# Kernel optimization log

Hardware: AMD Instinct MI355X
Metric: run time of the kernel (lower is better)

The kernel has to match this reference:

```python
import jax, jax.numpy as jnp
import numpy as np

H = 1024          # hidden_size
NH = 16           # num_attention_heads
HD = H // NH      # attention_head_size = 64
B, S = 8, 1024
LN_EPS = 1e-12


def setup_inputs() -> dict:
    key = jax.random.key(0)
    ks = jax.random.split(key, 12)
    sc = 0.02
    return {
        "input_tensor": jax.random.normal(ks[0], (B, S, H), dtype=jnp.float32),
        "attention_mask": jnp.zeros((B, S), dtype=jnp.float32),
        # LinearMem params (quantization disabled -> plain Linear, torch layout [out,in])
        "Wq": jax.random.normal(ks[1], (H, H), dtype=jnp.float32) * sc,
        "bq": jnp.zeros((H,), dtype=jnp.float32),
        "Wk": jax.random.normal(ks[2], (H, H), dtype=jnp.float32) * sc,
        "bk": jnp.zeros((H,), dtype=jnp.float32),
        "Wv": jax.random.normal(ks[3], (H, H), dtype=jnp.float32) * sc,
        "bv": jnp.zeros((H,), dtype=jnp.float32),
        "Wo": jax.random.normal(ks[4], (H, H), dtype=jnp.float32) * sc,
        "bo": jnp.zeros((H,), dtype=jnp.float32),
        "ln_gamma": jnp.ones((H,), dtype=jnp.float32),
        "ln_beta": jnp.zeros((H,), dtype=jnp.float32),
    }


def _heads(x):  # [B,S,H] -> [B,NH,S,HD]
    return x.reshape(B, S, NH, HD).transpose(0, 2, 1, 3)


def reference(input_tensor, attention_mask, Wq, bq, Wk, bk, Wv, bv, Wo, bo, ln_gamma, ln_beta):
    # Q/K/V projections (LinearMem with quantization disabled == Linear)
    q = _heads(jnp.einsum('bsh,oh->bso', input_tensor, Wq) + bq)
    k = _heads(jnp.einsum('bsh,oh->bso', input_tensor, Wk) + bk)
    v = _heads(jnp.einsum('bsh,oh->bso', input_tensor, Wv) + bv)
    scores = jnp.einsum('bnqd,bnkd->bnqk', q, k) / np.float32(np.sqrt(HD))
    scores = scores + attention_mask[:, None, None, :]  # additive mask [B,1,1,S]
    probs = jax.nn.softmax(scores, axis=-1)  # dropout = identity in eval
    ctx = jnp.einsum('bnqk,bnkd->bnqd', probs, v)
    ctx = ctx.transpose(0, 2, 1, 3).reshape(B, S, H)
    # output projection + residual LayerNorm (eps=1e-12)
    out = jnp.einsum('bsh,oh->bso', ctx, Wo) + bo
    resid = out + input_tensor
    mu = jnp.mean(resid, axis=-1, keepdims=True)
    var = jnp.mean(jnp.square(resid - mu), axis=-1, keepdims=True)
    return (resid - mu) * jax.lax.rsqrt(var + LN_EPS) * ln_gamma + ln_beta
```

## Files before the change

### kernel.cpp

```cpp
#include <hip/hip_runtime.h>

#define NHh 16

typedef unsigned short ushortT;
typedef __attribute__((ext_vector_type(8))) short short8;
typedef __attribute__((ext_vector_type(4))) float floatx4;

__device__ __forceinline__ ushortT f2bf(float x) {
    union { float f; unsigned int u; } cv; cv.f = x;
    unsigned int u = cv.u;
    unsigned int r = u + 0x7fffu + ((u >> 16) & 1u);
    return (ushortT)(r >> 16);
}

__device__ __forceinline__ unsigned pack2_trunc(float a, float b) {
    union { float f; unsigned u; } ua, ub;
    ua.f = a; ub.f = b;
    return (ub.u & 0xffff0000u) | (ua.u >> 16);
}

__device__ __forceinline__ void gload_lds16(const ushortT* g, ushortT* l) {
    __builtin_amdgcn_global_load_lds(
        (const __attribute__((address_space(1))) void*)g,
        (__attribute__((address_space(3))) void*)l, 16, 0, 0);
}

__global__ __launch_bounds__(256) void cvt_x(const float* __restrict__ in,
                                             ushortT* __restrict__ out, int n4) {
    int i = blockIdx.x * 256 + threadIdx.x;
    if (i >= n4) return;
    float4 f = ((const float4*)in)[i];
    uint2 o;
    o.x = (unsigned)f2bf(f.x) | ((unsigned)f2bf(f.y) << 16);
    o.y = (unsigned)f2bf(f.z) | ((unsigned)f2bf(f.w) << 16);
    ((uint2*)out)[i] = o;
}

__global__ __launch_bounds__(256) void cvt_w(const float* __restrict__ W0, const float* __restrict__ W1,
                                             const float* __restrict__ W2, const float* __restrict__ W3,
                                             ushortT* __restrict__ o0, ushortT* __restrict__ o1,
                                             ushortT* __restrict__ o2, ushortT* __restrict__ o3, int n4) {
    int z = blockIdx.y;
    const float* in = (z == 0) ? W0 : (z == 1) ? W1 : (z == 2) ? W2 : W3;
    ushortT* out = (z == 0) ? o0 : (z == 1) ? o1 : (z == 2) ? o2 : o3;
    int i = blockIdx.x * 256 + threadIdx.x;
    if (i >= n4) return;
    float4 f = ((const float4*)in)[i];
    uint2 o;
    o.x = (unsigned)f2bf(f.x) | ((unsigned)f2bf(f.y) << 16);
    o.y = (unsigned)f2bf(f.z) | ((unsigned)f2bf(f.w) << 16);
    ((uint2*)out)[i] = o;
}

__device__ __forceinline__ short8 lds_frag(const ushortT* tb, int row, int ks, int qd) {
    int rowblk = row >> 4;
    int r = row & 15;
    int c2 = qd ^ ((r >> 3) << 1);
    return *(const short8*)((const char*)tb + rowblk * 2048 + ks * 1024 + r * 64 + c2 * 16);
}

__global__ __launch_bounds__(512, 2) void qkv256(
        const ushortT* __restrict__ X,
        const ushortT* __restrict__ W0, const ushortT* __restrict__ W1, const ushortT* __restrict__ W2,
        const float* __restrict__ b0, const float* __restrict__ b1, const float* __restrict__ b2,
        ushortT* __restrict__ Qo, ushortT* __restrict__ Ko, ushortT* __restrict__ Vo) {
    __shared__ __align__(16) ushortT As[2 * 16384];
    __shared__ __align__(16) ushortT Bs[2 * 16384];

    const int l = blockIdx.x;
    const int z = l >> 7;
    const int idx = l & 127;
    const int tid = threadIdx.x;
    const int lane = tid & 63;
    const int w = tid >> 6;
    const int wr = w >> 2;
    const int wc = w & 3;
    const int qd = lane >> 4;
    const int ln = lane & 15;

    const ushortT* Ap; const ushortT* Bp;
    int arow0, brow0;
    if (z == 2) { Ap = W2; arow0 = (idx & 3) * 256; Bp = X; brow0 = (idx >> 2) * 256; }
    else { Ap = X; arow0 = (idx >> 2) * 256; Bp = (z == 0) ? W0 : W1; brow0 = (idx & 3) * 256; }

    floatx4 acc[8][4];
#pragma unroll
    for (int i = 0; i < 8; i++)
#pragma unroll
        for (int j = 0; j < 4; j++) acc[i][j] = (floatx4){0.f, 0.f, 0.f, 0.f};

    auto STAGE = [&](int cursor) {
        int kt = cursor >> 2;
        if (kt >= 16) return;
        int h = cursor & 3;
        int buf = kt & 1;
        int k0 = kt << 6;
        const ushortT* G = (h < 2) ? Ap : Bp;
        int row0 = (h < 2) ? arow0 : brow0;
        ushortT* L = (h < 2) ? (As + buf * 16384) : (Bs + buf * 16384);
        int half = h & 1;
#pragma unroll
        for (int j = 0; j < 2; j++) {
            int o = half * 16384 + j * 8192 + tid * 16;
            int rowblk = o >> 11;
            int colblk = (o >> 10) & 1;
            int r = (o >> 6) & 15;
            int c2 = ((o >> 4) & 3) ^ ((r >> 3) << 1);
            gload_lds16(G + (size_t)(row0 + rowblk * 16 + r) * 1024 + k0 + colblk * 32 + c2 * 8,
                        (ushortT*)((char*)L + o));
        }
    };

    for (int c = 0; c < 7; c++) STAGE(c);
    asm volatile("s_waitcnt vmcnt(6)" ::: "memory");
    __builtin_amdgcn_s_barrier();

    short8 afr[4][2], bfr[2][2];
    int cursor = 7;
    for (int T = 0; T < 16; T++) {
        const ushortT* Ab = As + (T & 1) * 16384;
        const ushortT* Bb = Bs + (T & 1) * 16384;
#pragma unroll
        for (int ph = 0; ph < 4; ph++) {
            const int mq = ph >> 1, nq = ph & 1;
#pragma unroll
            for (int ni = 0; ni < 2; ni++)
#pragma unroll
                for (int ks = 0; ks < 2; ks++)
                    bfr[ni][ks] = lds_frag(Bb, nq * 128 + ni * 64 + wc * 16 + ln, ks, qd);
            if (nq == 0) {
#pragma unroll
                for (int mi = 0; mi < 4; mi++)
#pragma unroll
                    for (int ks = 0; ks < 2; ks++)
                        afr[mi][ks] = lds_frag(Ab, (mq * 4 + mi) * 32 + wr * 16 + ln, ks, qd);
            }
            STAGE(cursor); ++cursor;
            __builtin_amdgcn_s_barrier();
            asm volatile("s_waitcnt lgkmcnt(0)" ::: "memory");
            __builtin_amdgcn_s_setprio(1);
#pragma unroll
            for (int mi = 0; mi < 4; mi++)
#pragma unroll
                for (int ni = 0; ni < 2; ni++)
#pragma unroll
                    for (int ks = 0; ks < 2; ks++)
                        acc[mq * 4 + mi][nq * 2 + ni] =
                            __builtin_amdgcn_mfma_f32_16x16x32_bf16(afr[mi][ks], bfr[ni][ks],
                                                                    acc[mq * 4 + mi][nq * 2 + ni], 0, 0, 0);
            __builtin_amdgcn_s_setprio(0);
            if (ph == 3) {
                if (T < 14) { asm volatile("s_waitcnt vmcnt(6)" ::: "memory"); }
                else        { asm volatile("s_waitcnt vmcnt(0)" ::: "memory"); }
            }
            __builtin_amdgcn_s_barrier();
        }
    }

    if (z == 2) {
        floatx4 bv4[8];
#pragma unroll
        for (int mi = 0; mi < 8; mi++)
            bv4[mi] = *(const floatx4*)(b2 + arow0 + mi * 32 + wr * 16 + qd * 4);
#pragma unroll
        for (int ni = 0; ni < 4; ni++) {
            int n = brow0 + ni * 64 + wc * 16 + ln;
            int bb = n >> 10, s = n & 1023;
#pragma unroll
            for (int mi = 0; mi < 8; mi++) {
#pragma unroll
                for (int r2 = 0; r2 < 4; r2++) {
                    int dim = arow0 + mi * 32 + wr * 16 + qd * 4 + r2;
                    int hh = dim >> 6, dd = dim & 63;
                    Vo[((size_t)(bb * NHh + hh) * 64 + dd) * 1024 + s] =
                        f2bf(acc[mi][ni][r2] + bv4[mi][r2]);
                }
            }
        }
    } else {
        ushortT* Out = z ? Ko : Qo;
        const float* bias = z ? b1 : b0;
#pragma unroll
        for (int ni = 0; ni < 4; ni++) {
            int n = brow0 + ni * 64 + wc * 16 + ln;
            float bb = bias[n];
            int h = n >> 6, d = n & 63;
#pragma unroll
            for (int mi = 0; mi < 8; mi++) {
#pragma unroll
                for (int r2 = 0; r2 < 4; r2++) {
                    int m = arow0 + mi * 32 + wr * 16 + qd * 4 + r2;
                    int b = m >> 10, s = m & 1023;
                    Out[(size_t)((b * NHh + h) * 1024 + s) * 64 + d] =
                        f2bf(acc[mi][ni][r2] + bb);
                }
            }
        }
    }
}

__global__ __launch_bounds__(256) void oproj_gemm(const ushortT* __restrict__ A,
        const ushortT* __restrict__ Wt, const float* __restrict__ bias, float* __restrict__ Pj) {
    __shared__ ushortT As[128 * 32];
    __shared__ ushortT Bs[128 * 32];
    const int l = blockIdx.x;
    const int m0 = (l & 63) * 128;
    const int n0 = (l >> 6) * 128;
    const int tid = threadIdx.x;
    const int lane = tid & 63;
    const int w = tid >> 6;
    const int qd = lane >> 4;
    const int ln = lane & 15;
    const int RM = (w >> 1) * 64;
    const int RN = (w & 1) * 64;

    floatx4 acc[4][4];
#pragma unroll
    for (int i = 0; i < 4; i++)
#pragma unroll
        for (int j = 0; j < 4; j++) acc[i][j] = (floatx4){0.f, 0.f, 0.f, 0.f};

    const int c0 = tid, c1 = tid + 256;
    for (int k0 = 0; k0 < 1024; k0 += 32) {
        gload_lds16(A + (size_t)(m0 + (c0 >> 2)) * 1024 + k0 + (c0 & 3) * 8, As + c0 * 8);
        gload_lds16(A + (size_t)(m0 + (c1 >> 2)) * 1024 + k0 + (c1 & 3) * 8, As + c1 * 8);
        gload_lds16(Wt + (size_t)(n0 + (c0 >> 2)) * 1024 + k0 + (c0 & 3) * 8, Bs + c0 * 8);
        gload_lds16(Wt + (size_t)(n0 + (c1 >> 2)) * 1024 + k0 + (c1 & 3) * 8, Bs + c1 * 8);
        __syncthreads();
        short8 af[4], bf8[4];
#pragma unroll
        for (int i = 0; i < 4; i++) af[i] = *(const short8*)&As[(RM + i * 16 + ln) * 32 + qd * 8];
#pragma unroll
        for (int j = 0; j < 4; j++) bf8[j] = *(const short8*)&Bs[(RN + j * 16 + ln) * 32 + qd * 8];
#pragma unroll
        for (int i = 0; i < 4; i++)
#pragma unroll
            for (int j = 0; j < 4; j++)
                acc[i][j] = __builtin_amdgcn_mfma_f32_16x16x32_bf16(af[i], bf8[j], acc[i][j], 0, 0, 0);
        __syncthreads();
    }

#pragma unroll
    for (int j = 0; j < 4; j++) {
        int n = n0 + RN + j * 16 + ln;
        float bb = bias[n];
#pragma unroll
        for (int i = 0; i < 4; i++) {
#pragma unroll
            for (int r2 = 0; r2 < 4; r2++) {
                int m = m0 + RM + i * 16 + qd * 4 + r2;
                Pj[(size_t)m * 1024 + n] = acc[i][j][r2] + bb;
            }
        }
    }
}

__global__ __launch_bounds__(256, 2) void attn_kernel(const ushortT* __restrict__ Q,
        const ushortT* __restrict__ K, const ushortT* __restrict__ Vg_t,
        const float* __restrict__ mask, ushortT* __restrict__ ctx) {
    __shared__ __align__(16) ushortT Ks[128 * 64];
    __shared__ __align__(16) ushortT Vt[64 * 128];
    __shared__ __align__(16) ushortT Ps[4][64 * 72];

    const int tid = threadIdx.x;
    const int lane = tid & 63;
    const int w = tid >> 6;
    const int qd = lane >> 4;
    const int ln = lane & 15;
    const int l = blockIdx.x;
    const int bh = l & 127;
    const int b = bh >> 4;
    const int h = bh & 15;
    const int qb = l >> 7;

    const ushortT* Qg = Q + (size_t)bh * 65536;
    const ushortT* Kg = K + (size_t)bh * 65536;
    const ushortT* Vg = Vg_t + (size_t)bh * 65536;
    const float* mrow = mask + b * 1024;
    const float LOG2E = 1.4426950408889634f;
    const float SCL = 0.125f * 1.4426950408889634f;

    short8 qf[4][2];
#pragma unroll
    for (int nj = 0; nj < 4; nj++)
#pragma unroll
        for (int ks = 0; ks < 2; ks++)
            qf[nj][ks] = *(const short8*)(Qg + (size_t)(qb * 256 + w * 64 + nj * 16 + ln) * 64 + ks * 32 + qd * 8);

    float lst[4] = {0.f, 0.f, 0.f, 0.f};
    floatx4 accO[4][4];
#pragma unroll
    for (int i = 0; i < 4; i++)
#pragma unroll
        for (int j = 0; j < 4; j++) accO[i][j] = (floatx4){0.f, 0.f, 0.f, 0.f};

    const int ksr = lane >> 3;
    const int kc  = lane & 7;
    const int vdr = lane >> 4;
    const int vcc = lane & 15;

    for (int kt = 0; kt < 8; ++kt) {
        __syncthreads();

#pragma unroll
        for (int ii = 0; ii < 4; ii++) {
            int i = w * 4 + ii;
            int srow = i * 8 + ksr;
            gload_lds16(Kg + (size_t)(kt * 128 + srow) * 64 + (kc ^ ksr) * 8,
                        Ks + i * 512 + lane * 8);
        }
#pragma unroll
        for (int ii = 0; ii < 4; ii++) {
            int i = w * 4 + ii;
            int d = i * 4 + vdr;
            gload_lds16(Vg + (size_t)d * 1024 + kt * 128 + (vcc ^ (d & 15)) * 8,
                        Vt + i * 512 + lane * 8);
        }

        __syncthreads();

#pragma unroll
        for (int h2 = 0; h2 < 2; ++h2) {
            const int s0g = kt * 128 + h2 * 64;

#pragma unroll
            for (int njp = 0; njp < 2; ++njp) {
                floatx4 sv[4][2];
#pragma unroll
                for (int mi = 0; mi < 4; mi++)
#pragma unroll
                    for (int j = 0; j < 2; j++) sv[mi][j] = (floatx4){0.f, 0.f, 0.f, 0.f};
#pragma unroll
                for (int ks = 0; ks < 2; ks++) {
                    short8 af[4];
#pragma unroll
                    for (int mi = 0; mi < 4; mi++)
                        af[mi] = *(const short8*)&Ks[(h2 * 64 + mi * 16 + ln) * 64 +
                                                     (((ks * 4 + qd) ^ (ln & 7)) * 8)];
#pragma unroll
                    for (int mi = 0; mi < 4; mi++)
#pragma unroll
                        for (int j = 0; j < 2; j++)
                            sv[mi][j] = __builtin_amdgcn_mfma_f32_16x16x32_bf16(af[mi], qf[njp * 2 + j][ks], sv[mi][j], 0, 0, 0);
                }

                float rs0 = 0.f, rs1 = 0.f;
#pragma unroll
                for (int mi = 0; mi < 4; mi++) {
                    floatx4 m4 = *(const floatx4*)(mrow + s0g + mi * 16 + qd * 4);
                    float p00 = __builtin_amdgcn_exp2f(sv[mi][0][0] * SCL + m4[0] * LOG2E);
                    float p01 = __builtin_amdgcn_exp2f(sv[mi][0][1] * SCL + m4[1] * LOG2E);
                    float p02 = __builtin_amdgcn_exp2f(sv[mi][0][2] * SCL + m4[2] * LOG2E);
                    float p03 = __builtin_amdgcn_exp2f(sv[mi][0][3] * SCL + m4[3] * LOG2E);
                    float p10 = __builtin_amdgcn_exp2f(sv[mi][1][0] * SCL + m4[0] * LOG2E);
                    float p11 = __builtin_amdgcn_exp2f(sv[mi][1][1] * SCL + m4[1] * LOG2E);
                    float p12 = __builtin_amdgcn_exp2f(sv[mi][1][2] * SCL + m4[2] * LOG2E);
                    float p13 = __builtin_amdgcn_exp2f(sv[mi][1][3] * SCL + m4[3] * LOG2E);
                    rs0 += (p00 + p01) + (p02 + p03);
                    rs1 += (p10 + p11) + (p12 + p13);
                    uint2 w0, w1;
                    w0.x = pack2_trunc(p00, p01); w0.y = pack2_trunc(p02, p03);
                    w1.x = pack2_trunc(p10, p11); w1.y = pack2_trunc(p12, p13);
                    *(uint2*)&Ps[w][(njp * 32 + ln) * 72 + mi * 16 + qd * 4] = w0;
                    *(uint2*)&Ps[w][(njp * 32 + 16 + ln) * 72 + mi * 16 + qd * 4] = w1;
                }
                rs0 += __shfl_xor(rs0, 16, 64); rs0 += __shfl_xor(rs0, 32, 64);
                rs1 += __shfl_xor(rs1, 16, 64); rs1 += __shfl_xor(rs1, 32, 64);
                lst[njp * 2 + 0] += rs0;
                lst[njp * 2 + 1] += rs1;
            }

#pragma unroll
            for (int ks2 = 0; ks2 < 2; ks2++) {
                short8 ap[4], bv[4];
#pragma unroll
                for (int i = 0; i < 4; i++)
                    ap[i] = *(const short8*)&Ps[w][(i * 16 + ln) * 72 + ks2 * 32 + qd * 8];
#pragma unroll
                for (int j = 0; j < 4; j++)
                    bv[j] = *(const short8*)&Vt[(j * 16 + ln) * 128 +
                                                (((h2 * 8 + ks2 * 4 + qd) ^ ln) * 8)];
#pragma unroll
                for (int i = 0; i < 4; i++)
#pragma unroll
                    for (int j = 0; j < 4; j++)
                        accO[i][j] = __builtin_amdgcn_mfma_f32_16x16x32_bf16(ap[i], bv[j], accO[i][j], 0, 0, 0);
            }
        }
    }

#pragma unroll
    for (int i = 0; i < 4; i++) {
#pragma unroll
        for (int r = 0; r < 4; r++) {
            float lv = __shfl(lst[i], qd * 4 + r, 64);
            float linv = 1.f / lv;
            int q = qb * 256 + w * 64 + i * 16 + qd * 4 + r;
#pragma unroll
            for (int j = 0; j < 4; j++) {
                int d = j * 16 + ln;
                ctx[((size_t)(b * 1024 + q)) * 1024 + h * 64 + d] = f2bf(accO[i][j][r] * linv);
            }
        }
    }
}

__global__ __launch_bounds__(256) void ln_kernel(const float* __restrict__ Pj, const float* __restrict__ X,
        const float* __restrict__ gamma, const float* __restrict__ beta, float* __restrict__ out) {
    __shared__ float red[8];
    int row = blockIdx.x;
    int t = threadIdx.x;
    const float4 p4 = ((const float4*)(Pj + (size_t)row * 1024))[t];
    const float4 x4 = ((const float4*)(X + (size_t)row * 1024))[t];
    float r0 = p4.x + x4.x, r1 = p4.y + x4.y, r2 = p4.z + x4.z, r3 = p4.w + x4.w;
    float s = r0 + r1 + r2 + r3;
    float ss = r0 * r0 + r1 * r1 + r2 * r2 + r3 * r3;
#pragma unroll
    for (int o = 1; o < 64; o <<= 1) { s += __shfl_xor(s, o, 64); ss += __shfl_xor(ss, o, 64); }
    int w = t >> 6;
    if ((t & 63) == 0) { red[w] = s; red[4 + w] = ss; }
    __syncthreads();
    s = red[0] + red[1] + red[2] + red[3];
    ss = red[4] + red[5] + red[6] + red[7];
    float mu = s * (1.f / 1024.f);
    float var = ss * (1.f / 1024.f) - mu * mu;
    float inv = rsqrtf(var + 1e-12f);
    const float4 g4 = ((const float4*)gamma)[t];
    const float4 b4 = ((const float4*)beta)[t];
    float4 o4;
    o4.x = (r0 - mu) * inv * g4.x + b4.x;
    o4.y = (r1 - mu) * inv * g4.y + b4.y;
    o4.z = (r2 - mu) * inv * g4.z + b4.z;
    o4.w = (r3 - mu) * inv * g4.w + b4.w;
    ((float4*)(out + (size_t)row * 1024))[t] = o4;
}

extern "C" void kernel_launch(void* const* d_in, const int* in_sizes, int n_in,
                              void* d_out, int out_size, void* d_ws, size_t ws_size,
                              hipStream_t stream) {
    const float* x     = (const float*)d_in[0];
    const float* mask  = (const float*)d_in[1];
    const float* Wq    = (const float*)d_in[2];
    const float* bq    = (const float*)d_in[3];
    const float* Wk    = (const float*)d_in[4];
    const float* bk    = (const float*)d_in[5];
    const float* Wv    = (const float*)d_in[6];
    const float* bv    = (const float*)d_in[7];
    const float* Wo    = (const float*)d_in[8];
    const float* bo    = (const float*)d_in[9];
    const float* gamma = (const float*)d_in[10];
    const float* beta  = (const float*)d_in[11];
    float* out = (float*)d_out;

    char* ws = (char*)d_ws;
    ushortT* Xb  = (ushortT*)(ws);
    ushortT* Wqb = (ushortT*)(ws + (16u << 20));
    ushortT* Wkb = (ushortT*)(ws + (18u << 20));
    ushortT* Wvb = (ushortT*)(ws + (20u << 20));
    ushortT* Wob = (ushortT*)(ws + (22u << 20));
    ushortT* Qb  = (ushortT*)(ws + (24u << 20));
    ushortT* Kb  = (ushortT*)(ws + (40u << 20));
    ushortT* Vb  = (ushortT*)(ws + (56u << 20));
    ushortT* Cb  = (ushortT*)(ws);
    float*   Pj  = (float*)(ws + (24u << 20));

    cvt_x<<<8192, 256, 0, stream>>>(x, Xb, 2097152);
    cvt_w<<<dim3(1024, 4), 256, 0, stream>>>(Wq, Wk, Wv, Wo, Wqb, Wkb, Wvb, Wob, 262144);
    qkv256<<<384, 512, 0, stream>>>(Xb, Wqb, Wkb, Wvb, bq, bk, bv, Qb, Kb, Vb);
    attn_kernel<<<512, 256, 0, stream>>>(Qb, Kb, Vb, mask, Cb);
    oproj_gemm<<<512, 256, 0, stream>>>(Cb, Wob, bo, Pj);
    ln_kernel<<<8192, 256, 0, stream>>>(Pj, x, gamma, beta, out);
}
```

Baseline: 292.5 us.

## Share a 256x128 pipelined GEMM loop between QKV and output projection with XCD-aware tiling

Moves the double-buffered, swizzled 8-wave MFMA main loop into a shared 256x128-tile helper. The QKV projection now launches 768 blocks with smaller tiles instead of 384 blocks of 256x256, and block indices are mapped so that blocks sharing an X row-panel land on the same XCD. The output projection moves from a simple single-buffered 128x128 kernel to this pipelined loop with the same XCD-aware mapping. The aim is better load balance across CUs, better L2 reuse, and latency hiding in the output GEMM, at the cost of lower per-block arithmetic intensity in QKV and a 256-block grid for the output projection.

```diff
diff --git a/kernel.cpp b/kernel.cpp
--- a/kernel.cpp
+++ b/kernel.cpp
@@ -59,67 +59,45 @@
     return *(const short8*)((const char*)tb + rowblk * 2048 + ks * 1024 + r * 64 + c2 * 16);
 }
 
-__global__ __launch_bounds__(512, 2) void qkv256(
-        const ushortT* __restrict__ X,
-        const ushortT* __restrict__ W0, const ushortT* __restrict__ W1, const ushortT* __restrict__ W2,
-        const float* __restrict__ b0, const float* __restrict__ b1, const float* __restrict__ b2,
-        ushortT* __restrict__ Qo, ushortT* __restrict__ Ko, ushortT* __restrict__ Vo) {
-    __shared__ __align__(16) ushortT As[2 * 16384];
-    __shared__ __align__(16) ushortT Bs[2 * 16384];
-
-    const int l = blockIdx.x;
-    const int z = l >> 7;
-    const int idx = l & 127;
-    const int tid = threadIdx.x;
-    const int lane = tid & 63;
-    const int w = tid >> 6;
-    const int wr = w >> 2;
-    const int wc = w & 3;
-    const int qd = lane >> 4;
-    const int ln = lane & 15;
-
-    const ushortT* Ap; const ushortT* Bp;
-    int arow0, brow0;
-    if (z == 2) { Ap = W2; arow0 = (idx & 3) * 256; Bp = X; brow0 = (idx >> 2) * 256; }
-    else { Ap = X; arow0 = (idx >> 2) * 256; Bp = (z == 0) ? W0 : W1; brow0 = (idx & 3) * 256; }
-
-    floatx4 acc[8][4];
-#pragma unroll
-    for (int i = 0; i < 8; i++)
-#pragma unroll
-        for (int j = 0; j < 4; j++) acc[i][j] = (floatx4){0.f, 0.f, 0.f, 0.f};
-
+__device__ __forceinline__ void gemm_loop_256x128(
+        const ushortT* __restrict__ Ap, const ushortT* __restrict__ Bp,
+        int arow0, int brow0, ushortT* As, ushortT* Bs,
+        int tid, int wr, int wc, int qd, int ln, floatx4 (&acc)[4][4]) {
     auto STAGE = [&](int cursor) {
         int kt = cursor >> 2;
         if (kt >= 16) return;
         int h = cursor & 3;
         int buf = kt & 1;
         int k0 = kt << 6;
-        const ushortT* G = (h < 2) ? Ap : Bp;
-        int row0 = (h < 2) ? arow0 : brow0;
-        ushortT* L = (h < 2) ? (As + buf * 16384) : (Bs + buf * 16384);
-        int half = h & 1;
-#pragma unroll
-        for (int j = 0; j < 2; j++) {
-            int o = half * 16384 + j * 8192 + tid * 16;
-            int rowblk = o >> 11;
-            int colblk = (o >> 10) & 1;
-            int r = (o >> 6) & 15;
+        if (h < 2) {
+            char* L = (char*)As + buf * 32768;
+#pragma unroll
+            for (int jj = 0; jj < 2; jj++) {
+                int o = h * 16384 + jj * 8192 + tid * 16;
+                int rowblk = o >> 11, ks = (o >> 10) & 1, r = (o >> 6) & 15;
+                int c2 = ((o >> 4) & 3) ^ ((r >> 3) << 1);
+                gload_lds16(Ap + (size_t)(arow0 + rowblk * 16 + r) * 1024 + k0 + ks * 32 + c2 * 8,
+                            (ushortT*)(L + o));
+            }
+        } else {
+            char* L = (char*)Bs + buf * 16384;
+            int o = (h & 1) * 8192 + tid * 16;
+            int rowblk = o >> 11, ks = (o >> 10) & 1, r = (o >> 6) & 15;
             int c2 = ((o >> 4) & 3) ^ ((r >> 3) << 1);
-            gload_lds16(G + (size_t)(row0 + rowblk * 16 + r) * 1024 + k0 + colblk * 32 + c2 * 8,
-                        (ushortT*)((char*)L + o));
+            gload_lds16(Bp + (size_t)(brow0 + rowblk * 16 + r) * 1024 + k0 + ks * 32 + c2 * 8,
+                        (ushortT*)(L + o));
         }
     };
 
     for (int c = 0; c < 7; c++) STAGE(c);
-    asm volatile("s_waitcnt vmcnt(6)" ::: "memory");
+    asm volatile("s_waitcnt vmcnt(5)" ::: "memory");
     __builtin_amdgcn_s_barrier();
 
-    short8 afr[4][2], bfr[2][2];
+    short8 afr[2][2], bfr[2][2];
     int cursor = 7;
     for (int T = 0; T < 16; T++) {
         const ushortT* Ab = As + (T & 1) * 16384;
-        const ushortT* Bb = Bs + (T & 1) * 16384;
+        const ushortT* Bb = Bs + (T & 1) * 8192;
 #pragma unroll
         for (int ph = 0; ph < 4; ph++) {
             const int mq = ph >> 1, nq = ph & 1;
@@ -127,50 +105,93 @@
             for (int ni = 0; ni < 2; ni++)
 #pragma unroll
                 for (int ks = 0; ks < 2; ks++)
-                    bfr[ni][ks] = lds_frag(Bb, nq * 128 + ni * 64 + wc * 16 + ln, ks, qd);
+                    bfr[ni][ks] = lds_frag(Bb, nq * 64 + ni * 32 + wc * 16 + ln, ks, qd);
             if (nq == 0) {
 #pragma unroll
-                for (int mi = 0; mi < 4; mi++)
+                for (int mi = 0; mi < 2; mi++)
 #pragma unroll
                     for (int ks = 0; ks < 2; ks++)
-                        afr[mi][ks] = lds_frag(Ab, (mq * 4 + mi) * 32 + wr * 16 + ln, ks, qd);
+                        afr[mi][ks] = lds_frag(Ab, (mq * 2 + mi) * 64 + wr * 16 + ln, ks, qd);
             }
             STAGE(cursor); ++cursor;
             __builtin_amdgcn_s_barrier();
             asm volatile("s_waitcnt lgkmcnt(0)" ::: "memory");
             __builtin_amdgcn_s_setprio(1);
 #pragma unroll
-            for (int mi = 0; mi < 4; mi++)
+            for (int mi = 0; mi < 2; mi++)
 #pragma unroll
                 for (int ni = 0; ni < 2; ni++)
 #pragma unroll
                     for (int ks = 0; ks < 2; ks++)
-                        acc[mq * 4 + mi][nq * 2 + ni] =
+                        acc[mq * 2 + mi][nq * 2 + ni] =
                             __builtin_amdgcn_mfma_f32_16x16x32_bf16(afr[mi][ks], bfr[ni][ks],
-                                                                    acc[mq * 4 + mi][nq * 2 + ni], 0, 0, 0);
+                                                                    acc[mq * 2 + mi][nq * 2 + ni], 0, 0, 0);
             __builtin_amdgcn_s_setprio(0);
             if (ph == 3) {
-                if (T < 14) { asm volatile("s_waitcnt vmcnt(6)" ::: "memory"); }
+                if (T < 14) { asm volatile("s_waitcnt vmcnt(5)" ::: "memory"); }
                 else        { asm volatile("s_waitcnt vmcnt(0)" ::: "memory"); }
             }
             __builtin_amdgcn_s_barrier();
         }
     }
+}
+
+__global__ __launch_bounds__(512, 1) void qkv_gemm8(
+        const ushortT* __restrict__ X,
+        const ushortT* __restrict__ W0, const ushortT* __restrict__ W1, const ushortT* __restrict__ W2,
+        const float* __restrict__ b0, const float* __restrict__ b1, const float* __restrict__ b2,
+        ushortT* __restrict__ Qo, ushortT* __restrict__ Ko, ushortT* __restrict__ Vo) {
+    __shared__ __align__(16) ushortT As[2 * 16384];
+    __shared__ __align__(16) ushortT Bs[2 * 8192];
+
+    const int l = blockIdx.x;
+    const int xcd = l & 7;
+    const int j = l >> 3;
+    const int tid = threadIdx.x;
+    const int lane = tid & 63;
+    const int w = tid >> 6;
+    const int wr = w >> 1, wc = w & 1;
+    const int qd = lane >> 4, ln = lane & 15;
+
+    int z, arow0, brow0;
+    const ushortT* Ap; const ushortT* Bp;
+    if (j < 64) {
+        z = j >> 5;
+        int mg = (j >> 3) & 3;
+        int n = j & 7;
+        arow0 = (mg * 8 + xcd) * 256;
+        brow0 = n * 128;
+        Ap = X; Bp = z ? W1 : W0;
+    } else {
+        z = 2;
+        int j2 = j - 64;
+        arow0 = (j2 & 3) * 256;
+        brow0 = ((j2 >> 2) * 8 + xcd) * 128;
+        Ap = W2; Bp = X;
+    }
+
+    floatx4 acc[4][4];
+#pragma unroll
+    for (int i = 0; i < 4; i++)
+#pragma unroll
+        for (int jj = 0; jj < 4; jj++) acc[i][jj] = (floatx4){0.f, 0.f, 0.f, 0.f};
+
+    gemm_loop_256x128(Ap, Bp, arow0, brow0, As, Bs, tid, wr, wc, qd, ln, acc);
 
     if (z == 2) {
-        floatx4 bv4[8];
-#pragma unroll
-        for (int mi = 0; mi < 8; mi++)
-            bv4[mi] = *(const floatx4*)(b2 + arow0 + mi * 32 + wr * 16 + qd * 4);
+        floatx4 bv4[4];
+#pragma unroll
+        for (int mi = 0; mi < 4; mi++)
+            bv4[mi] = *(const floatx4*)(b2 + arow0 + mi * 64 + wr * 16 + qd * 4);
 #pragma unroll
         for (int ni = 0; ni < 4; ni++) {
-            int n = brow0 + ni * 64 + wc * 16 + ln;
+            int n = brow0 + ni * 32 + wc * 16 + ln;
             int bb = n >> 10, s = n & 1023;
 #pragma unroll
-            for (int mi = 0; mi < 8; mi++) {
+            for (int mi = 0; mi < 4; mi++) {
 #pragma unroll
                 for (int r2 = 0; r2 < 4; r2++) {
-                    int dim = arow0 + mi * 32 + wr * 16 + qd * 4 + r2;
+                    int dim = arow0 + mi * 64 + wr * 16 + qd * 4 + r2;
                     int hh = dim >> 6, dd = dim & 63;
                     Vo[((size_t)(bb * NHh + hh) * 64 + dd) * 1024 + s] =
                         f2bf(acc[mi][ni][r2] + bv4[mi][r2]);
@@ -182,14 +203,14 @@
         const float* bias = z ? b1 : b0;
 #pragma unroll
         for (int ni = 0; ni < 4; ni++) {
-            int n = brow0 + ni * 64 + wc * 16 + ln;
+            int n = brow0 + ni * 32 + wc * 16 + ln;
             float bb = bias[n];
             int h = n >> 6, d = n & 63;
 #pragma unroll
-            for (int mi = 0; mi < 8; mi++) {
+            for (int mi = 0; mi < 4; mi++) {
 #pragma unroll
                 for (int r2 = 0; r2 < 4; r2++) {
-                    int m = arow0 + mi * 32 + wr * 16 + qd * 4 + r2;
+                    int m = arow0 + mi * 64 + wr * 16 + qd * 4 + r2;
                     int b = m >> 10, s = m & 1023;
                     Out[(size_t)((b * NHh + h) * 1024 + s) * 64 + d] =
                         f2bf(acc[mi][ni][r2] + bb);
@@ -199,57 +220,41 @@
     }
 }
 
-__global__ __launch_bounds__(256) void oproj_gemm(const ushortT* __restrict__ A,
+__global__ __launch_bounds__(512, 1) void oproj_gemm8(const ushortT* __restrict__ A,
         const ushortT* __restrict__ Wt, const float* __restrict__ bias, float* __restrict__ Pj) {
-    __shared__ ushortT As[128 * 32];
-    __shared__ ushortT Bs[128 * 32];
+    __shared__ __align__(16) ushortT As[2 * 16384];
+    __shared__ __align__(16) ushortT Bs[2 * 8192];
+
     const int l = blockIdx.x;
-    const int m0 = (l & 63) * 128;
-    const int n0 = (l >> 6) * 128;
+    const int xcd = l & 7;
+    const int j = l >> 3;
     const int tid = threadIdx.x;
     const int lane = tid & 63;
     const int w = tid >> 6;
-    const int qd = lane >> 4;
-    const int ln = lane & 15;
-    const int RM = (w >> 1) * 64;
-    const int RN = (w & 1) * 64;
+    const int wr = w >> 1, wc = w & 1;
+    const int qd = lane >> 4, ln = lane & 15;
+
+    const int arow0 = ((j & 3) * 8 + xcd) * 256;
+    const int brow0 = (j >> 2) * 128;
 
     floatx4 acc[4][4];
 #pragma unroll
     for (int i = 0; i < 4; i++)
 #pragma unroll
-        for (int j = 0; j < 4; j++) acc[i][j] = (floatx4){0.f, 0.f, 0.f, 0.f};
-
-    const int c0 = tid, c1 = tid + 256;
-    for (int k0 = 0; k0 < 1024; k0 += 32) {
-        gload_lds16(A + (size_t)(m0 + (c0 >> 2)) * 1024 + k0 + (c0 & 3) * 8, As + c0 * 8);
-        gload_lds16(A + (size_t)(m0 + (c1 >> 2)) * 1024 + k0 + (c1 & 3) * 8, As + c1 * 8);
-        gload_lds16(Wt + (size_t)(n0 + (c0 >> 2)) * 1024 + k0 + (c0 & 3) * 8, Bs + c0 * 8);
-        gload_lds16(Wt + (size_t)(n0 + (c1 >> 2)) * 1024 + k0 + (c1 & 3) * 8, Bs + c1 * 8);
-        __syncthreads();
-        short8 af[4], bf8[4];
-#pragma unroll
-        for (int i = 0; i < 4; i++) af[i] = *(const short8*)&As[(RM + i * 16 + ln) * 32 + qd * 8];
-#pragma unroll
-        for (int j = 0; j < 4; j++) bf8[j] = *(const short8*)&Bs[(RN + j * 16 + ln) * 32 + qd * 8];
-#pragma unroll
-        for (int i = 0; i < 4; i++)
-#pragma unroll
-            for (int j = 0; j < 4; j++)
-                acc[i][j] = __builtin_amdgcn_mfma_f32_16x16x32_bf16(af[i], bf8[j], acc[i][j], 0, 0, 0);
-        __syncthreads();
-    }
-
-#pragma unroll
-    for (int j = 0; j < 4; j++) {
-        int n = n0 + RN + j * 16 + ln;
+        for (int jj = 0; jj < 4; jj++) acc[i][jj] = (floatx4){0.f, 0.f, 0.f, 0.f};
+
+    gemm_loop_256x128(A, Wt, arow0, brow0, As, Bs, tid, wr, wc, qd, ln, acc);
+
+#pragma unroll
+    for (int ni = 0; ni < 4; ni++) {
+        int n = brow0 + ni * 32 + wc * 16 + ln;
         float bb = bias[n];
 #pragma unroll
-        for (int i = 0; i < 4; i++) {
+        for (int mi = 0; mi < 4; mi++) {
 #pragma unroll
             for (int r2 = 0; r2 < 4; r2++) {
-                int m = m0 + RM + i * 16 + qd * 4 + r2;
-                Pj[(size_t)m * 1024 + n] = acc[i][j][r2] + bb;
+                int m = arow0 + mi * 64 + wr * 16 + qd * 4 + r2;
+                Pj[(size_t)m * 1024 + n] = acc[mi][ni][r2] + bb;
             }
         }
     }
@@ -466,8 +471,8 @@
 
     cvt_x<<<8192, 256, 0, stream>>>(x, Xb, 2097152);
     cvt_w<<<dim3(1024, 4), 256, 0, stream>>>(Wq, Wk, Wv, Wo, Wqb, Wkb, Wvb, Wob, 262144);
-    qkv256<<<384, 512, 0, stream>>>(Xb, Wqb, Wkb, Wvb, bq, bk, bv, Qb, Kb, Vb);
+    qkv_gemm8<<<768, 512, 0, stream>>>(Xb, Wqb, Wkb, Wvb, bq, bk, bv, Qb, Kb, Vb);
     attn_kernel<<<512, 256, 0, stream>>>(Qb, Kb, Vb, mask, Cb);
-    oproj_gemm<<<512, 256, 0, stream>>>(Cb, Wob, bo, Pj);
+    oproj_gemm8<<<256, 512, 0, stream>>>(Cb, Wob, bo, Pj);
     ln_kernel<<<8192, 256, 0, stream>>>(Pj, x, gamma, beta, out);
 }
```

After: 299.4 us. 1.02x slower.
